# Kernel tuning notes

Hardware: AMD Instinct MI355X
Metric: run time of the kernel (lower is better)

The kernel has to match this reference:

```python
import jax, jax.numpy as jnp
import numpy as np

DIM = 768
HEADS = 12
HEAD_DIM = DIM // HEADS
B, S = 2, 2048
EPS = 1e-5


def _layernorm(x, w, b):
    mu = jnp.mean(x, axis=-1, keepdims=True)
    var = jnp.mean(jnp.square(x - mu), axis=-1, keepdims=True)
    return (x - mu) * jax.lax.rsqrt(var + EPS) * w + b


def setup_inputs() -> dict:
    key = jax.random.key(0)
    ks = jax.random.split(key, 16)
    sc = 1.0 / np.sqrt(DIM)
    inp = {
        'x': jax.random.normal(ks[0], (B, S, DIM), jnp.float32),
        'bias': jax.random.normal(ks[1], (HEADS, B, S, S), jnp.float32),
        'mask': jax.random.randint(ks[2], (1, B, S, S), 0, 2, jnp.int32),
        'ln1_w': jnp.ones((DIM,), jnp.float32),
        'ln1_b': jnp.zeros((DIM,), jnp.float32),
        'wq': jax.random.normal(ks[3], (DIM, DIM), jnp.float32) * sc,
        'bq': jnp.zeros((DIM,), jnp.float32),
        'wk': jax.random.normal(ks[4], (DIM, DIM), jnp.float32) * sc,
        'bk': jnp.zeros((DIM,), jnp.float32),
        'wv': jax.random.normal(ks[5], (DIM, DIM), jnp.float32) * sc,
        'bv': jnp.zeros((DIM,), jnp.float32),
        'wo': jax.random.normal(ks[6], (DIM, DIM), jnp.float32) * sc,
        'bo': jnp.zeros((DIM,), jnp.float32),
        'ln2_w': jnp.ones((DIM,), jnp.float32),
        'ln2_b': jnp.zeros((DIM,), jnp.float32),
        'w1': jax.random.normal(ks[7], (DIM, DIM), jnp.float32) * sc,
        'b1': jnp.zeros((DIM,), jnp.float32),
        'w2': jax.random.normal(ks[8], (DIM, DIM), jnp.float32) * sc,
        'b2': jnp.zeros((DIM,), jnp.float32),
    }
    return inp


def _split_heads(t):
    # [B,S,D] -> [H,B,S,Dh]  (matches torch view + permute(2,0,1,3))
    return t.reshape(B, S, HEADS, HEAD_DIM).transpose(2, 0, 1, 3)


def reference(x, bias, mask, ln1_w, ln1_b, wq, bq, wk, bk, wv, bv, wo, bo,
              ln2_w, ln2_b, w1, b1, w2, b2):
    xn = _layernorm(x, ln1_w, ln1_b)
    q = _split_heads(xn @ wq + bq)
    k = _split_heads(xn @ wk + bk)
    v = _split_heads(xn @ wv + bv)
    # scores: [H,B,Sq,Sk]; bias added BEFORE scaling, then masked, then scaled softmax
    scores = jnp.einsum('hbqd,hbkd->hbqk', q, k) + bias
    scores = jnp.where(mask == 0, jnp.float32(-1e20), scores)
    probs = jax.nn.softmax(scores / np.sqrt(HEAD_DIM), axis=-1)
    attn = jnp.einsum('hbqk,hbkd->hbqd', probs, v)
    attn = attn.transpose(1, 2, 0, 3).reshape(B, S, DIM)
    x = x + (attn @ wo + bo)
    xn = _layernorm(x, ln2_w, ln2_b)
    h = jax.nn.relu(xn @ w1 + b1)
    x = x + (h @ w2 + b2)
    return x
```

## Files before the change

### kernel.cpp

```cpp
#include <hip/hip_runtime.h>
#include <math.h>

#define DIMM 768
#define SEQ 2048
#define BATB 2
#define NHEAD 12
#define DHEAD 64
#define ROWS 4096

typedef __attribute__((ext_vector_type(8))) short bf16x8;
typedef __attribute__((ext_vector_type(4))) float f32x4;
typedef unsigned short ushort_t;
typedef unsigned int uint_t;

union U16 { int4 i; ushort_t u[8]; };

__device__ __forceinline__ ushort_t f2b(float f) {
    uint_t u = __float_as_uint(f);
    return (ushort_t)((u + 0x7FFFu + ((u >> 16) & 1u)) >> 16);
}

__device__ __forceinline__ void gl16(const ushort_t* g, ushort_t* l) {
    __builtin_amdgcn_global_load_lds(
        (const __attribute__((address_space(1))) unsigned int*)g,
        (__attribute__((address_space(3))) unsigned int*)l,
        16, 0, 0);
}

struct WPtrs { const float* s[6]; };
struct BPtrs { const float* p[3]; };

__global__ __launch_bounds__(256) void wtrans_k(WPtrs wp, ushort_t* __restrict__ dst)
{
    __shared__ float T[64][65];
    int wi = blockIdx.z;
    const float* in = wp.s[wi];
    ushort_t* out = dst + (size_t)wi * (DIMM * DIMM);
    int kb = blockIdx.y * 64, nb = blockIdx.x * 64;
    int t = threadIdx.x;
    int kl = t >> 4, nl = (t & 15) * 4;
    #pragma unroll
    for (int it = 0; it < 4; it++) {
        float4 a = *(const float4*)&in[(size_t)(kb + kl + it * 16) * DIMM + nb + nl];
        T[kl + it * 16][nl + 0] = a.x;
        T[kl + it * 16][nl + 1] = a.y;
        T[kl + it * 16][nl + 2] = a.z;
        T[kl + it * 16][nl + 3] = a.w;
    }
    __syncthreads();
    int no = t >> 2, ko = (t & 3) * 16;
    #pragma unroll
    for (int j = 0; j < 2; j++) {
        U16 u;
        #pragma unroll
        for (int c = 0; c < 8; c++) u.u[c] = f2b(T[ko + j * 8 + c][no]);
        *(int4*)&out[(size_t)(nb + no) * DIMM + kb + ko + j * 8] = u.i;
    }
}

__global__ __launch_bounds__(256) void ln_k(const float* __restrict__ x,
                                            const float* __restrict__ w,
                                            const float* __restrict__ b,
                                            ushort_t* __restrict__ out)
{
    int row = blockIdx.x;
    int tid = threadIdx.x;
    const float* xr = x + (size_t)row * DIMM;
    float v0 = xr[tid], v1 = xr[tid + 256], v2 = xr[tid + 512];
    float s  = v0 + v1 + v2;
    float ss = v0 * v0 + v1 * v1 + v2 * v2;
    #pragma unroll
    for (int off = 32; off > 0; off >>= 1) {
        s  += __shfl_down(s,  off);
        ss += __shfl_down(ss, off);
    }
    __shared__ float ws_[4], wss_[4];
    __shared__ float mu_s, rs_s;
    int lane = tid & 63, wid = tid >> 6;
    if (lane == 0) { ws_[wid] = s; wss_[wid] = ss; }
    __syncthreads();
    if (tid == 0) {
        float S1 = ws_[0] + ws_[1] + ws_[2] + ws_[3];
        float S2 = wss_[0] + wss_[1] + wss_[2] + wss_[3];
        float m = S1 * (1.0f / DIMM);
        float var = S2 * (1.0f / DIMM) - m * m;
        mu_s = m;
        rs_s = rsqrtf(var + 1e-5f);
    }
    __syncthreads();
    float mu = mu_s, rs = rs_s;
    ushort_t* orow = out + (size_t)row * DIMM;
    orow[tid]       = f2b((v0 - mu) * rs * w[tid]       + b[tid]);
    orow[tid + 256] = f2b((v1 - mu) * rs * w[tid + 256] + b[tid + 256]);
    orow[tid + 512] = f2b((v2 - mu) * rs * w[tid + 512] + b[tid + 512]);
}

template<int ASRC, int OMODE, bool RELU, bool RES, int NB>
__global__ __launch_bounds__(256) void mgemm_k(const ushort_t* __restrict__ A,
                                               const ushort_t* __restrict__ BT,
                                               BPtrs bias,
                                               const float* __restrict__ res,
                                               void* __restrict__ outv)
{
    __shared__ alignas(16) ushort_t Asl[16 * 64 * 8];
    __shared__ alignas(16) ushort_t Bsl[16 * 64 * 8];
    int tid = threadIdx.x;
    int lane = tid & 63, w = tid >> 6;
    int wr = w >> 1, wc = w & 1;
    int colBase = blockIdx.x * 128, rowBase = blockIdx.y * 128;

    size_t offA[4], offB[4];
    ushort_t* dstA[4];
    ushort_t* dstB[4];
    const size_t strideA = (ASRC == 1) ? (size_t)64 : (size_t)BATB * SEQ * DHEAD;
    #pragma unroll
    for (int i = 0; i < 4; i++) {
        int s  = i * 4 + w;
        int mt = s >> 1, ks = s & 1;
        int rr = mt * 16 + (lane & 15);
        int kk = ks * 32 + (lane >> 4) * 8;
        if (ASRC == 1) {
            offA[i] = (size_t)(rowBase + rr) * DIMM + kk;
        } else {
            int r = rowBase + rr;
            offA[i] = ((size_t)(r >> 11) * SEQ + (r & 2047)) * DHEAD + kk;
        }
        dstA[i] = &Asl[(size_t)s * 64 * 8];
        offB[i] = (size_t)(colBase + rr) * DIMM + kk;
        dstB[i] = &Bsl[(size_t)s * 64 * 8];
    }

    f32x4 acc[4][4];
    #pragma unroll
    for (int mi = 0; mi < 4; mi++)
        #pragma unroll
        for (int ni = 0; ni < 4; ni++) { f32x4 z = {0.f, 0.f, 0.f, 0.f}; acc[mi][ni] = z; }

    for (int t = 0; t < DIMM / 64; t++) {
        #pragma unroll
        for (int i = 0; i < 4; i++) { gl16(A  + offA[i], dstA[i]); offA[i] += strideA; }
        #pragma unroll
        for (int i = 0; i < 4; i++) { gl16(BT + offB[i], dstB[i]); offB[i] += 64; }
        __syncthreads();
        bf16x8 b[4][2];
        #pragma unroll
        for (int ni = 0; ni < 4; ni++)
            #pragma unroll
            for (int ks = 0; ks < 2; ks++)
                b[ni][ks] = *(bf16x8*)&Bsl[((((wc * 4 + ni) * 2 + ks)) * 64 + lane) * 8];
        #pragma unroll
        for (int mi = 0; mi < 4; mi++) {
            bf16x8 a0 = *(bf16x8*)&Asl[((((wr * 4 + mi) * 2 + 0)) * 64 + lane) * 8];
            bf16x8 a1 = *(bf16x8*)&Asl[((((wr * 4 + mi) * 2 + 1)) * 64 + lane) * 8];
            #pragma unroll
            for (int ni = 0; ni < 4; ni++) {
                acc[mi][ni] = __builtin_amdgcn_mfma_f32_16x16x32_bf16(a0, b[ni][0], acc[mi][ni], 0, 0, 0);
                acc[mi][ni] = __builtin_amdgcn_mfma_f32_16x16x32_bf16(a1, b[ni][1], acc[mi][ni], 0, 0, 0);
            }
        }
        __syncthreads();
    }
    int wi = (NB == 3) ? (colBase / DIMM) : 0;
    const float* bp_ = bias.p[wi];
    int col_l = lane & 15, quad = lane >> 4;
    #pragma unroll
    for (int ni = 0; ni < 4; ni++) {
        int n = colBase + wc * 64 + ni * 16 + col_l;
        float bn = bp_[n - wi * DIMM];
        #pragma unroll
        for (int mi = 0; mi < 4; mi++) {
            #pragma unroll
            for (int r = 0; r < 4; r++) {
                int row = rowBase + wr * 64 + mi * 16 + quad * 4 + r;
                float v = acc[mi][ni][r] + bn;
                if (RELU) v = fmaxf(v, 0.0f);
                if (RES)  v += res[(size_t)row * DIMM + n];
                if (OMODE == 0) {
                    ((float*)outv)[(size_t)row * DIMM + n] = v;
                } else if (OMODE == 1) {
                    ((ushort_t*)outv)[(size_t)row * DIMM + n] = f2b(v);
                } else {
                    ((ushort_t*)outv)[((size_t)((n >> 6) * BATB + (row >> 11)) * SEQ + (row & 2047)) * DHEAD + (n & 63)] = f2b(v);
                }
            }
        }
    }
}

__global__ __launch_bounds__(256) void attn_k(const ushort_t* __restrict__ q,
                                              const ushort_t* __restrict__ k,
                                              const ushort_t* __restrict__ v,
                                              const float* __restrict__ bias,
                                              const int* __restrict__ mask,
                                              ushort_t* __restrict__ out)
{
    __shared__ alignas(16) ushort_t Kf[8 * 64 * 8];
    __shared__ alignas(16) ushort_t Vf[8 * 64 * 8];
    __shared__ alignas(16) ushort_t Pf[8 * 64 * 8];
    int tid = threadIdx.x, lane = tid & 63, w = tid >> 6;
    int col_l = lane & 15, quad = lane >> 4;
    int qbase = blockIdx.x * 64;
    int hb = blockIdx.y;
    const ushort_t* qp = q + (size_t)hb * SEQ * DHEAD;
    const ushort_t* kp = k + (size_t)hb * SEQ * DHEAD;
    const ushort_t* vp = v + (size_t)hb * SEQ * DHEAD;
    const float* bp = bias + (size_t)hb * SEQ * SEQ;
    const int*   mp = mask + (size_t)(hb & 1) * SEQ * SEQ;

    bf16x8 qF0 = *(const bf16x8*)&qp[(size_t)(qbase + w * 16 + col_l) * DHEAD + (quad * 8)];
    bf16x8 qF1 = *(const bf16x8*)&qp[(size_t)(qbase + w * 16 + col_l) * DHEAD + 32 + (quad * 8)];

    size_t offK[2];
    ushort_t* dstK[2];
    #pragma unroll
    for (int i = 0; i < 2; i++) {
        int slot = i * 4 + w;
        int sn = ((slot & 3) << 4) | (lane & 15);
        int c  = ((slot >> 2) << 2) | (lane >> 4);
        offK[i] = (size_t)sn * DHEAD + 8 * c;
        dstK[i] = &Kf[(size_t)(i * 256 + w * 64) * 8];
    }

    f32x4 O[4];
    #pragma unroll
    for (int nt = 0; nt < 4; nt++) { f32x4 z = {0.f, 0.f, 0.f, 0.f}; O[nt] = z; }
    float m_run[4], l_run[4];
    #pragma unroll
    for (int r = 0; r < 4; r++) { m_run[r] = -1e30f; l_run[r] = 0.0f; }

    int j0 = (tid >> 3) * 2, e0 = (tid & 7) * 8;
    const float C2 = 0.18033688011112042f;

    for (int kvb = 0; kvb < SEQ; kvb += 64) {
        gl16(kp + (size_t)kvb * DHEAD + offK[0], dstK[0]);
        gl16(kp + (size_t)kvb * DHEAD + offK[1], dstK[1]);
        {
            U16 g0, g1;
            g0.i = *(const int4*)&vp[(size_t)(kvb + j0) * DHEAD + e0];
            g1.i = *(const int4*)&vp[(size_t)(kvb + j0 + 1) * DHEAD + e0];
            int js = j0 >> 5, grp = (j0 & 31) >> 3, i0 = j0 & 7;
            #pragma unroll
            for (int c = 0; c < 8; c++) {
                int n = e0 + c;
                uint_t pk = (uint_t)g0.u[c] | ((uint_t)g1.u[c] << 16);
                int idx = ((js * 4 + (n >> 4)) * 64 + ((n & 15) | (grp << 4))) * 8 + i0;
                *(uint_t*)&Vf[idx] = pk;
            }
        }
        float bl[4][4]; int ml[4][4];
        #pragma unroll
        for (int nt = 0; nt < 4; nt++) {
            int col = kvb + nt * 16 + col_l;
            #pragma unroll
            for (int r = 0; r < 4; r++) {
                int qrow = qbase + w * 16 + quad * 4 + r;
                bl[nt][r] = bp[(size_t)qrow * SEQ + col];
                ml[nt][r] = mp[(size_t)qrow * SEQ + col];
            }
        }
        __syncthreads();
        f32x4 S[4];
        #pragma unroll
        for (int nt = 0; nt < 4; nt++) {
            bf16x8 b0 = *(bf16x8*)&Kf[((0 * 4 + nt) * 64 + lane) * 8];
            bf16x8 b1 = *(bf16x8*)&Kf[((1 * 4 + nt) * 64 + lane) * 8];
            f32x4 z = {0.f, 0.f, 0.f, 0.f};
            z = __builtin_amdgcn_mfma_f32_16x16x32_bf16(qF0, b0, z, 0, 0, 0);
            S[nt] = __builtin_amdgcn_mfma_f32_16x16x32_bf16(qF1, b1, z, 0, 0, 0);
        }
        float lg[4][4];
        #pragma unroll
        for (int nt = 0; nt < 4; nt++)
            #pragma unroll
            for (int r = 0; r < 4; r++)
                lg[nt][r] = ml[nt][r] ? (S[nt][r] + bl[nt][r]) * C2 : -2.0e18f;
        #pragma unroll
        for (int r = 0; r < 4; r++) {
            float mx = fmaxf(fmaxf(lg[0][r], lg[1][r]), fmaxf(lg[2][r], lg[3][r]));
            mx = fmaxf(mx, __shfl_xor(mx, 1));
            mx = fmaxf(mx, __shfl_xor(mx, 2));
            mx = fmaxf(mx, __shfl_xor(mx, 4));
            mx = fmaxf(mx, __shfl_xor(mx, 8));
            if (!__all(mx - m_run[r] <= 4.0f)) {
                float mnew = fmaxf(m_run[r], mx);
                float alpha = __builtin_amdgcn_exp2f(m_run[r] - mnew);
                m_run[r] = mnew;
                l_run[r] *= alpha;
                #pragma unroll
                for (int nt = 0; nt < 4; nt++) O[nt][r] *= alpha;
            }
            float mcur = m_run[r];
            float rs = 0.0f;
            #pragma unroll
            for (int nt = 0; nt < 4; nt++) {
                float pp = __builtin_amdgcn_exp2f(lg[nt][r] - mcur);
                lg[nt][r] = pp;
                rs += pp;
            }
            rs += __shfl_xor(rs, 1);
            rs += __shfl_xor(rs, 2);
            rs += __shfl_xor(rs, 4);
            rs += __shfl_xor(rs, 8);
            l_run[r] += rs;
        }
        #pragma unroll
        for (int nt = 0; nt < 4; nt++) {
            int j = nt * 16 + col_l;
            #pragma unroll
            for (int r = 0; r < 4; r++) {
                ushort_t pu = f2b(lg[nt][r]);
                uint_t po = (uint_t)(unsigned)__shfl_xor((int)pu, 1);
                if ((lane & 1) == 0) {
                    int m = quad * 4 + r;
                    int idx = ((w * 2 + (j >> 5)) * 64 + (m | (((j & 31) >> 3) << 4))) * 8 + (j & 7);
                    *(uint_t*)&Pf[idx] = (uint_t)pu | (po << 16);
                }
            }
        }
        #pragma unroll
        for (int jss = 0; jss < 2; jss++) {
            bf16x8 pF = *(bf16x8*)&Pf[((w * 2 + jss) * 64 + lane) * 8];
            #pragma unroll
            for (int nt = 0; nt < 4; nt++) {
                bf16x8 vF = *(bf16x8*)&Vf[((jss * 4 + nt) * 64 + lane) * 8];
                O[nt] = __builtin_amdgcn_mfma_f32_16x16x32_bf16(pF, vF, O[nt], 0, 0, 0);
            }
        }
        __syncthreads();
    }
    float inv[4];
    #pragma unroll
    for (int r = 0; r < 4; r++) inv[r] = 1.0f / l_run[r];
    #pragma unroll
    for (int nt = 0; nt < 4; nt++)
        #pragma unroll
        for (int r = 0; r < 4; r++) {
            int row = qbase + w * 16 + quad * 4 + r;
            out[((size_t)hb * SEQ + row) * DHEAD + nt * 16 + col_l] = f2b(O[nt][r] * inv[r]);
        }
}

extern "C" void kernel_launch(void* const* d_in, const int* in_sizes, int n_in,
                              void* d_out, int out_size, void* d_ws, size_t ws_size,
                              hipStream_t stream)
{
    const float* x    = (const float*)d_in[0];
    const float* bias = (const float*)d_in[1];
    const int*   mask = (const int*)d_in[2];
    const float* ln1w = (const float*)d_in[3];
    const float* ln1b = (const float*)d_in[4];
    const float* wq   = (const float*)d_in[5];
    const float* bq   = (const float*)d_in[6];
    const float* wk   = (const float*)d_in[7];
    const float* bk   = (const float*)d_in[8];
    const float* wv   = (const float*)d_in[9];
    const float* bv   = (const float*)d_in[10];
    const float* wo   = (const float*)d_in[11];
    const float* bo   = (const float*)d_in[12];
    const float* ln2w = (const float*)d_in[13];
    const float* ln2b = (const float*)d_in[14];
    const float* w1   = (const float*)d_in[15];
    const float* b1   = (const float*)d_in[16];
    const float* w2   = (const float*)d_in[17];
    const float* b2   = (const float*)d_in[18];

    const size_t WSZ = (size_t)DIMM * DIMM;
    const size_t ABUF = (size_t)ROWS * DIMM;

    ushort_t* wsu  = (ushort_t*)d_ws;
    ushort_t* wT   = wsu;
    ushort_t* qb   = wsu + 6 * WSZ;
    ushort_t* kbuf = qb + ABUF;
    ushort_t* vbuf = kbuf + ABUF;
    ushort_t* xn1  = vbuf + ABUF;
    float*    x1   = (float*)(xn1 + ABUF);
    ushort_t* hid  = qb;

    WPtrs wp; wp.s[0] = wq; wp.s[1] = wk; wp.s[2] = wv; wp.s[3] = wo; wp.s[4] = w1; wp.s[5] = w2;
    BPtrs bqkv; bqkv.p[0] = bq; bqkv.p[1] = bk; bqkv.p[2] = bv;
    BPtrs bbo;  bbo.p[0]  = bo; bbo.p[1]  = bo; bbo.p[2]  = bo;
    BPtrs bb1;  bb1.p[0]  = b1; bb1.p[1]  = b1; bb1.p[2]  = b1;
    BPtrs bb2;  bb2.p[0]  = b2; bb2.p[1]  = b2; bb2.p[2]  = b2;

    dim3 gg(6, 32), gb(256);
    wtrans_k<<<dim3(12, 12, 6), 256, 0, stream>>>(wp, wT);
    ln_k<<<ROWS, 256, 0, stream>>>(x, ln1w, ln1b, xn1);
    mgemm_k<1, 2, false, false, 3><<<dim3(18, 32), gb, 0, stream>>>(xn1, wT, bqkv, nullptr, qb);
    attn_k<<<dim3(32, 24), 256, 0, stream>>>(qb, kbuf, vbuf, bias, mask, xn1);
    mgemm_k<2, 0, false, true, 1><<<gg, gb, 0, stream>>>(xn1, wT + 3 * WSZ, bbo, x, x1);
    ln_k<<<ROWS, 256, 0, stream>>>(x1, ln2w, ln2b, xn1);
    mgemm_k<1, 1, true, false, 1><<<gg, gb, 0, stream>>>(xn1, wT + 4 * WSZ, bb1, nullptr, hid);
    mgemm_k<1, 0, false, true, 1><<<gg, gb, 0, stream>>>(hid, wT + 5 * WSZ, bb2, x1, (float*)d_out);
}
```

Measured before the change: 798.9 us.

## Double-buffer LDS tiles and prefetch bias, mask and V in GEMM and attention

The GEMM kernel now keeps two LDS buffers for A and B. It issues the global-to-LDS loads for the next K tile before running the MFMAs on the current one, and uses one barrier per iteration instead of two. The attention kernel also double-buffers K and V in LDS. It loads the next block's bias and mask into registers one iteration ahead and V two blocks ahead, so the large bias/mask stream overlaps with the MFMA and softmax work. In exchange it uses more LDS and more registers, which may lower occupancy, and it relies on hand-placed vmcnt/lgkmcnt waits for correctness.

```diff
diff --git a/kernel.cpp b/kernel.cpp
--- a/kernel.cpp
+++ b/kernel.cpp
@@ -102,16 +102,15 @@
                                                const float* __restrict__ res,
                                                void* __restrict__ outv)
 {
-    __shared__ alignas(16) ushort_t Asl[16 * 64 * 8];
-    __shared__ alignas(16) ushort_t Bsl[16 * 64 * 8];
+    __shared__ alignas(16) ushort_t Asl[2][16 * 64 * 8];
+    __shared__ alignas(16) ushort_t Bsl[2][16 * 64 * 8];
     int tid = threadIdx.x;
     int lane = tid & 63, w = tid >> 6;
     int wr = w >> 1, wc = w & 1;
     int colBase = blockIdx.x * 128, rowBase = blockIdx.y * 128;
 
     size_t offA[4], offB[4];
-    ushort_t* dstA[4];
-    ushort_t* dstB[4];
+    int lbA[4], lbB[4];
     const size_t strideA = (ASRC == 1) ? (size_t)64 : (size_t)BATB * SEQ * DHEAD;
     #pragma unroll
     for (int i = 0; i < 4; i++) {
@@ -125,9 +124,9 @@
             int r = rowBase + rr;
             offA[i] = ((size_t)(r >> 11) * SEQ + (r & 2047)) * DHEAD + kk;
         }
-        dstA[i] = &Asl[(size_t)s * 64 * 8];
+        lbA[i] = s * 64 * 8;
         offB[i] = (size_t)(colBase + rr) * DIMM + kk;
-        dstB[i] = &Bsl[(size_t)s * 64 * 8];
+        lbB[i] = s * 64 * 8;
     }
 
     f32x4 acc[4][4];
@@ -136,29 +135,42 @@
         #pragma unroll
         for (int ni = 0; ni < 4; ni++) { f32x4 z = {0.f, 0.f, 0.f, 0.f}; acc[mi][ni] = z; }
 
-    for (int t = 0; t < DIMM / 64; t++) {
-        #pragma unroll
-        for (int i = 0; i < 4; i++) { gl16(A  + offA[i], dstA[i]); offA[i] += strideA; }
-        #pragma unroll
-        for (int i = 0; i < 4; i++) { gl16(BT + offB[i], dstB[i]); offB[i] += 64; }
-        __syncthreads();
+    const int NT = DIMM / 64;
+    #pragma unroll
+    for (int i = 0; i < 4; i++) { gl16(A  + offA[i], &Asl[0][lbA[i]]); offA[i] += strideA; }
+    #pragma unroll
+    for (int i = 0; i < 4; i++) { gl16(BT + offB[i], &Bsl[0][lbB[i]]); offB[i] += 64; }
+    __syncthreads();
+
+    int p = 0;
+    for (int t = 0; t < NT; t++) {
+        if (t + 1 < NT) {
+            #pragma unroll
+            for (int i = 0; i < 4; i++) { gl16(A  + offA[i], &Asl[p ^ 1][lbA[i]]); offA[i] += strideA; }
+            #pragma unroll
+            for (int i = 0; i < 4; i++) { gl16(BT + offB[i], &Bsl[p ^ 1][lbB[i]]); offB[i] += 64; }
+        }
         bf16x8 b[4][2];
         #pragma unroll
         for (int ni = 0; ni < 4; ni++)
             #pragma unroll
             for (int ks = 0; ks < 2; ks++)
-                b[ni][ks] = *(bf16x8*)&Bsl[((((wc * 4 + ni) * 2 + ks)) * 64 + lane) * 8];
+                b[ni][ks] = *(bf16x8*)&Bsl[p][((((wc * 4 + ni) * 2 + ks)) * 64 + lane) * 8];
         #pragma unroll
         for (int mi = 0; mi < 4; mi++) {
-            bf16x8 a0 = *(bf16x8*)&Asl[((((wr * 4 + mi) * 2 + 0)) * 64 + lane) * 8];
-            bf16x8 a1 = *(bf16x8*)&Asl[((((wr * 4 + mi) * 2 + 1)) * 64 + lane) * 8];
+            bf16x8 a0 = *(bf16x8*)&Asl[p][((((wr * 4 + mi) * 2 + 0)) * 64 + lane) * 8];
+            bf16x8 a1 = *(bf16x8*)&Asl[p][((((wr * 4 + mi) * 2 + 1)) * 64 + lane) * 8];
             #pragma unroll
             for (int ni = 0; ni < 4; ni++) {
                 acc[mi][ni] = __builtin_amdgcn_mfma_f32_16x16x32_bf16(a0, b[ni][0], acc[mi][ni], 0, 0, 0);
                 acc[mi][ni] = __builtin_amdgcn_mfma_f32_16x16x32_bf16(a1, b[ni][1], acc[mi][ni], 0, 0, 0);
             }
         }
-        __syncthreads();
+        if (t + 1 < NT) {
+            asm volatile("s_waitcnt vmcnt(0)" ::: "memory");
+            __builtin_amdgcn_s_barrier();
+        }
+        p ^= 1;
     }
     int wi = (NB == 3) ? (colBase / DIMM) : 0;
     const float* bp_ = bias.p[wi];
@@ -194,8 +206,8 @@
                                               const int* __restrict__ mask,
                                               ushort_t* __restrict__ out)
 {
-    __shared__ alignas(16) ushort_t Kf[8 * 64 * 8];
-    __shared__ alignas(16) ushort_t Vf[8 * 64 * 8];
+    __shared__ alignas(16) ushort_t Kf[2][8 * 64 * 8];
+    __shared__ alignas(16) ushort_t Vf[2][8 * 64 * 8];
     __shared__ alignas(16) ushort_t Pf[8 * 64 * 8];
     int tid = threadIdx.x, lane = tid & 63, w = tid >> 6;
     int col_l = lane & 15, quad = lane >> 4;
@@ -210,16 +222,18 @@
     bf16x8 qF0 = *(const bf16x8*)&qp[(size_t)(qbase + w * 16 + col_l) * DHEAD + (quad * 8)];
     bf16x8 qF1 = *(const bf16x8*)&qp[(size_t)(qbase + w * 16 + col_l) * DHEAD + 32 + (quad * 8)];
 
-    size_t offK[2];
-    ushort_t* dstK[2];
+    size_t offK[2]; int lbK[2];
     #pragma unroll
     for (int i = 0; i < 2; i++) {
         int slot = i * 4 + w;
         int sn = ((slot & 3) << 4) | (lane & 15);
         int c  = ((slot >> 2) << 2) | (lane >> 4);
         offK[i] = (size_t)sn * DHEAD + 8 * c;
-        dstK[i] = &Kf[(size_t)(i * 256 + w * 64) * 8];
-    }
+        lbK[i] = (i * 256 + w * 64) * 8;
+    }
+    int j0 = (tid >> 3) * 2, e0 = (tid & 7) * 8;
+    int js = j0 >> 5, grp = (j0 & 31) >> 3, i0 = j0 & 7;
+    size_t voff = (size_t)j0 * DHEAD + e0;
 
     f32x4 O[4];
     #pragma unroll
@@ -228,42 +242,78 @@
     #pragma unroll
     for (int r = 0; r < 4; r++) { m_run[r] = -1e30f; l_run[r] = 0.0f; }
 
-    int j0 = (tid >> 3) * 2, e0 = (tid & 7) * 8;
     const float C2 = 0.18033688011112042f;
 
+    gl16(kp + offK[0], &Kf[0][lbK[0]]);
+    gl16(kp + offK[1], &Kf[0][lbK[1]]);
+    float blF[4][4]; int mlF[4][4];
+    #pragma unroll
+    for (int nt = 0; nt < 4; nt++) {
+        int col = nt * 16 + col_l;
+        #pragma unroll
+        for (int r = 0; r < 4; r++) {
+            int qrow = qbase + w * 16 + quad * 4 + r;
+            blF[nt][r] = bp[(size_t)qrow * SEQ + col];
+            mlF[nt][r] = mp[(size_t)qrow * SEQ + col];
+        }
+    }
+    int4 vr0 = *(const int4*)&vp[voff];
+    int4 vr1 = *(const int4*)&vp[voff + DHEAD];
+    {
+        U16 g0, g1; g0.i = vr0; g1.i = vr1;
+        #pragma unroll
+        for (int c = 0; c < 8; c++) {
+            int n = e0 + c;
+            uint_t pk = (uint_t)g0.u[c] | ((uint_t)g1.u[c] << 16);
+            int idx = ((js * 4 + (n >> 4)) * 64 + ((n & 15) | (grp << 4))) * 8 + i0;
+            *(uint_t*)&Vf[0][idx] = pk;
+        }
+    }
+    {
+        size_t b1 = (size_t)64 * DHEAD;
+        vr0 = *(const int4*)&vp[b1 + voff];
+        vr1 = *(const int4*)&vp[b1 + voff + DHEAD];
+    }
+    __syncthreads();
+
+    int p = 0;
     for (int kvb = 0; kvb < SEQ; kvb += 64) {
-        gl16(kp + (size_t)kvb * DHEAD + offK[0], dstK[0]);
-        gl16(kp + (size_t)kvb * DHEAD + offK[1], dstK[1]);
-        {
-            U16 g0, g1;
-            g0.i = *(const int4*)&vp[(size_t)(kvb + j0) * DHEAD + e0];
-            g1.i = *(const int4*)&vp[(size_t)(kvb + j0 + 1) * DHEAD + e0];
-            int js = j0 >> 5, grp = (j0 & 31) >> 3, i0 = j0 & 7;
+        asm volatile("s_waitcnt vmcnt(0)" ::: "memory");
+        if (kvb + 64 < SEQ) {
+            U16 g0, g1; g0.i = vr0; g1.i = vr1;
             #pragma unroll
             for (int c = 0; c < 8; c++) {
                 int n = e0 + c;
                 uint_t pk = (uint_t)g0.u[c] | ((uint_t)g1.u[c] << 16);
                 int idx = ((js * 4 + (n >> 4)) * 64 + ((n & 15) | (grp << 4))) * 8 + i0;
-                *(uint_t*)&Vf[idx] = pk;
-            }
-        }
-        float bl[4][4]; int ml[4][4];
+                *(uint_t*)&Vf[p ^ 1][idx] = pk;
+            }
+            gl16(kp + (size_t)(kvb + 64) * DHEAD + offK[0], &Kf[p ^ 1][lbK[0]]);
+            gl16(kp + (size_t)(kvb + 64) * DHEAD + offK[1], &Kf[p ^ 1][lbK[1]]);
+        }
+        float blN[4][4]; int mlN[4][4];
+        if (kvb + 64 < SEQ) {
+            #pragma unroll
+            for (int nt = 0; nt < 4; nt++) {
+                int col = kvb + 64 + nt * 16 + col_l;
+                #pragma unroll
+                for (int r = 0; r < 4; r++) {
+                    int qrow = qbase + w * 16 + quad * 4 + r;
+                    blN[nt][r] = bp[(size_t)qrow * SEQ + col];
+                    mlN[nt][r] = mp[(size_t)qrow * SEQ + col];
+                }
+            }
+        }
+        if (kvb + 128 < SEQ) {
+            size_t b2 = (size_t)(kvb + 128) * DHEAD;
+            vr0 = *(const int4*)&vp[b2 + voff];
+            vr1 = *(const int4*)&vp[b2 + voff + DHEAD];
+        }
+        f32x4 S[4];
         #pragma unroll
         for (int nt = 0; nt < 4; nt++) {
-            int col = kvb + nt * 16 + col_l;
-            #pragma unroll
-            for (int r = 0; r < 4; r++) {
-                int qrow = qbase + w * 16 + quad * 4 + r;
-                bl[nt][r] = bp[(size_t)qrow * SEQ + col];
-                ml[nt][r] = mp[(size_t)qrow * SEQ + col];
-            }
-        }
-        __syncthreads();
-        f32x4 S[4];
-        #pragma unroll
-        for (int nt = 0; nt < 4; nt++) {
-            bf16x8 b0 = *(bf16x8*)&Kf[((0 * 4 + nt) * 64 + lane) * 8];
-            bf16x8 b1 = *(bf16x8*)&Kf[((1 * 4 + nt) * 64 + lane) * 8];
+            bf16x8 b0 = *(bf16x8*)&Kf[p][((0 * 4 + nt) * 64 + lane) * 8];
+            bf16x8 b1 = *(bf16x8*)&Kf[p][((1 * 4 + nt) * 64 + lane) * 8];
             f32x4 z = {0.f, 0.f, 0.f, 0.f};
             z = __builtin_amdgcn_mfma_f32_16x16x32_bf16(qF0, b0, z, 0, 0, 0);
             S[nt] = __builtin_amdgcn_mfma_f32_16x16x32_bf16(qF1, b1, z, 0, 0, 0);
@@ -273,7 +323,7 @@
         for (int nt = 0; nt < 4; nt++)
             #pragma unroll
             for (int r = 0; r < 4; r++)
-                lg[nt][r] = ml[nt][r] ? (S[nt][r] + bl[nt][r]) * C2 : -2.0e18f;
+                lg[nt][r] = mlF[nt][r] ? (S[nt][r] + blF[nt][r]) * C2 : -2.0e18f;
         #pragma unroll
         for (int r = 0; r < 4; r++) {
             float mx = fmaxf(fmaxf(lg[0][r], lg[1][r]), fmaxf(lg[2][r], lg[3][r]));
@@ -322,11 +372,20 @@
             bf16x8 pF = *(bf16x8*)&Pf[((w * 2 + jss) * 64 + lane) * 8];
             #pragma unroll
             for (int nt = 0; nt < 4; nt++) {
-                bf16x8 vF = *(bf16x8*)&Vf[((jss * 4 + nt) * 64 + lane) * 8];
+                bf16x8 vF = *(bf16x8*)&Vf[p][((jss * 4 + nt) * 64 + lane) * 8];
                 O[nt] = __builtin_amdgcn_mfma_f32_16x16x32_bf16(pF, vF, O[nt], 0, 0, 0);
             }
         }
-        __syncthreads();
+        #pragma unroll
+        for (int nt = 0; nt < 4; nt++)
+            #pragma unroll
+            for (int r = 0; r < 4; r++) { blF[nt][r] = blN[nt][r]; mlF[nt][r] = mlN[nt][r]; }
+        if (kvb + 64 < SEQ) {
+            asm volatile("s_waitcnt vmcnt(2)" ::: "memory");
+            asm volatile("s_waitcnt lgkmcnt(0)" ::: "memory");
+            __builtin_amdgcn_s_barrier();
+        }
+        p ^= 1;
     }
     float inv[4];
     #pragma unroll
```

Result: slower. 882.5 us (+10.5%).
